# Optimization experiments

Hardware: AMD Instinct MI355X
Metric: run time of the kernel (lower is better)

The kernel has to match this reference:

```python
import jax, jax.numpy as jnp
import numpy as np

N, E, T, F, HID, NCLS = 50000, 800000, 6, 64, 48, 2
LN_EPS = 1e-5


def setup_inputs() -> dict:
    key = jax.random.key(0)
    ks = jax.random.split(key, 24)
    p = lambda k, shape, s=0.1: jax.random.normal(k, shape, dtype=jnp.float32) * s
    inp = {
        "x_seq": jax.random.normal(ks[0], (T, N, F), dtype=jnp.float32),
        "edge_index": jax.random.randint(ks[1], (2, E), 0, N, dtype=jnp.int64),
        "edge_weight": jax.random.uniform(ks[2], (E,), dtype=jnp.float32),
        # GCN layer 0
        "W0": p(ks[3], (F, HID)), "b0": jnp.zeros((HID,), jnp.float32),
        "g0": jnp.ones((HID,), jnp.float32), "be0": jnp.zeros((HID,), jnp.float32),
        # GCN layer 1
        "W1": p(ks[4], (HID, HID)), "b1": jnp.zeros((HID,), jnp.float32),
        "g1": jnp.ones((HID,), jnp.float32), "be1": jnp.zeros((HID,), jnp.float32),
        # GRU (torch gate order: r, z, n)
        "W_ih": p(ks[5], (3 * HID, HID)), "W_hh": p(ks[6], (3 * HID, HID)),
        "b_ih": jnp.zeros((3 * HID,), jnp.float32), "b_hh": jnp.zeros((3 * HID,), jnp.float32),
        # classifier MLP
        "Wc1": p(ks[7], (HID, HID // 2)), "bc1": jnp.zeros((HID // 2,), jnp.float32),
        "Wc2": p(ks[8], (HID // 2, NCLS)), "bc2": jnp.zeros((NCLS,), jnp.float32),
    }
    return inp


def _layer_norm(x, g, b):
    mu = x.mean(-1, keepdims=True)
    var = ((x - mu) ** 2).mean(-1, keepdims=True)
    return (x - mu) * jax.lax.rsqrt(var + LN_EPS) * g + b


def reference(x_seq, edge_index, edge_weight, W0, b0, g0, be0, W1, b1, g1, be1,
              W_ih, W_hh, b_ih, b_hh, Wc1, bc1, Wc2, bc2):
    n = x_seq.shape[1]
    hid = W0.shape[1]
    row, col = edge_index[0], edge_index[1]
    # PyG GCNConv default: add self-loops (weight 1), symmetric normalization
    loop = jnp.arange(n)
    row_f = jnp.concatenate([row, loop])
    col_f = jnp.concatenate([col, loop])
    w_f = jnp.concatenate([edge_weight, jnp.ones((n,), edge_weight.dtype)])
    deg = jax.ops.segment_sum(w_f, col_f, num_segments=n)
    dis = jnp.where(deg > 0, jax.lax.rsqrt(jnp.maximum(deg, 1e-12)), 0.0)
    norm = dis[row_f] * w_f * dis[col_f]  # [E+N]

    def gcn(x, W, b):
        h = x @ W                              # [N, hid]
        msg = h[row_f] * norm[:, None]         # [E+N, hid]
        return jax.ops.segment_sum(msg, col_f, num_segments=n) + b

    def spatial(x_t):
        # layer 0: no residual (in_dim != hid)
        h1 = jax.nn.relu(_layer_norm(gcn(x_t, W0, b0), g0, be0))
        # layer 1: residual (dropout is eval-mode no-op)
        h2 = jax.nn.relu(_layer_norm(gcn(h1, W1, b1), g1, be1)) + h1
        return h2

    # sequential map over T keeps per-step [E,hid] message buffers small
    H = jax.lax.map(spatial, x_seq)            # [T, N, hid]

    def gru_step(h, x_t):
        gi = x_t @ W_ih.T + b_ih               # [N, 3*hid]
        gh = h @ W_hh.T + b_hh
        i_r, i_z, i_n = jnp.split(gi, 3, axis=-1)
        h_r, h_z, h_n = jnp.split(gh, 3, axis=-1)
        r = jax.nn.sigmoid(i_r + h_r)
        z = jax.nn.sigmoid(i_z + h_z)
        nv = jnp.tanh(i_n + r * h_n)
        h_new = (1.0 - z) * nv + z * h
        return h_new, None

    h0 = jnp.zeros((n, hid), x_seq.dtype)
    z_last, _ = jax.lax.scan(gru_step, h0, H)  # last hidden state [N, hid]

    logits = jax.nn.relu(z_last @ Wc1 + bc1) @ Wc2 + bc2  # [N, 2]
    return logits
```

## Files before the change

kernel.cpp:

```cpp
#include <hip/hip_runtime.h>
#include <hip/hip_fp16.h>
#include <math.h>

#define NN 50000
#define NE 800000
#define TT 6
#define HID 48
#define NB 196

__device__ __forceinline__ float sigmoidf_(float x){ return 1.0f/(1.0f+__expf(-x)); }
__device__ __forceinline__ float tanhf_(float x){
  float xc = fminf(fmaxf(x,-15.f),15.f);
  float t = __expf(2.f*xc);
  return (t-1.f)/(t+1.f);
}
__device__ __forceinline__ unsigned f2bf(float x){
  unsigned u = __float_as_uint(x);
  return (u + 0x7fffu + ((u>>16)&1u)) >> 16;
}
__device__ __forceinline__ unsigned pack2(float a, float b){
  return f2bf(a) | (f2bf(b)<<16);
}
__device__ __forceinline__ float bflo(unsigned u){ return __uint_as_float(u<<16); }
__device__ __forceinline__ float bfhi(unsigned u){ return __uint_as_float(u & 0xffff0000u); }
__device__ __forceinline__ unsigned f2h(float x){
  return (unsigned)__half_as_ushort(__float2half(x));
}
__device__ __forceinline__ float h2f(unsigned u){
  return __half2float(__ushort_as_half((unsigned short)(u & 0xffffu)));
}
__device__ __forceinline__ unsigned pack2h(float a, float b){
  return f2h(a) | (f2h(b)<<16);
}

typedef __fp16 h2t __attribute__((ext_vector_type(2)));

__device__ __forceinline__ unsigned pkrtz(float a, float b){
#if __has_builtin(__builtin_amdgcn_cvt_pkrtz)
  auto r = __builtin_amdgcn_cvt_pkrtz(a, b);
  return __builtin_bit_cast(unsigned, r);
#else
  return pack2h(a, b);
#endif
}
__device__ __forceinline__ float dot2f(unsigned a, unsigned b, float c){
#if __has_builtin(__builtin_amdgcn_fdot2)
  return __builtin_amdgcn_fdot2(__builtin_bit_cast(h2t, a), __builtin_bit_cast(h2t, b), c, false);
#else
  h2t av = __builtin_bit_cast(h2t, a), bv = __builtin_bit_cast(h2t, b);
  return c + (float)av[0]*(float)bv[0] + (float)av[1]*(float)bv[1];
#endif
}

struct U3 { unsigned x,y,z; };

__device__ __forceinline__ int block_scan_incl(int x, int* wsum){
  int lane = threadIdx.x & 63, w = threadIdx.x >> 6;
  int v = x;
#pragma unroll
  for(int d=1; d<64; d<<=1){
    int u = __shfl_up(v, d, 64);
    if(lane >= d) v += u;
  }
  if(lane==63) wsum[w] = v;
  __syncthreads();
  int add = 0;
#pragma unroll
  for(int k=0;k<3;k++) if(w>k) add += wsum[k];
  return v + add;
}

__global__ __launch_bounds__(256) void k_setup(int* cnt,
                                               const float* __restrict__ Wih, const float* __restrict__ Whh,
                                               unsigned* Wall){
  int i = blockIdx.x*256+threadIdx.x;
  if(i<NN) cnt[i]=0;
  if(i < 6*24*48){
    int wv = i/1152, r = i%1152;
    int k2 = r/48, c = r%48;
    int cc = (c<24)? c : (c-24);
    int row = (cc<8) ? (wv*8 + cc) : (cc<16) ? (48 + wv*8 + cc-8) : (96 + wv*8 + cc-16);
    const float* Wsrc = (c<24)? Whh : Wih;
    Wall[i] = pack2h(Wsrc[row*48 + 2*k2], Wsrc[row*48 + 2*k2 + 1]);
  }
}

__global__ __launch_bounds__(256) void k_cnt(const int* __restrict__ ei, int* cnt, int* pos){
  int e = blockIdx.x*256+threadIdx.x;
  if(e<NE){
    int c = ei[NE+e];
    pos[e] = atomicAdd(&cnt[c], 1);
  }
}

__global__ __launch_bounds__(256) void k_partA(const int* __restrict__ cnt, int* bsum){
  __shared__ int wsum[4];
  int i = blockIdx.x*256+threadIdx.x;
  int x = (i<NN)? cnt[i] : 0;
  int lane = threadIdx.x & 63, w = threadIdx.x >> 6;
  int v = x;
#pragma unroll
  for(int m=32;m>=1;m>>=1) v += __shfl_xor(v, m, 64);
  if(lane==0) wsum[w]=v;
  __syncthreads();
  if(threadIdx.x==0) bsum[blockIdx.x] = wsum[0]+wsum[1]+wsum[2]+wsum[3];
}

__global__ __launch_bounds__(256) void k_midB(const int* __restrict__ bsum, int* bpre, int* offs){
  __shared__ int wsum[4];
  int t = threadIdx.x;
  int x = (t<NB)? bsum[t] : 0;
  int incl = block_scan_incl(x, wsum);
  if(t<NB) bpre[t] = incl - x;
  if(t==255) offs[NN] = incl;
}

__global__ __launch_bounds__(256) void k_offsC(const int* __restrict__ cnt, const int* __restrict__ bpre,
                                               int* offs){
  __shared__ int wsum[4];
  int i = blockIdx.x*256+threadIdx.x;
  int x = (i<NN)? cnt[i] : 0;
  int incl = block_scan_incl(x, wsum);
  if(i<NN) offs[i] = bpre[blockIdx.x] + incl - x;
}

__global__ __launch_bounds__(256) void k_scatter(const int* __restrict__ ei, const float* __restrict__ ew,
                                                 const int* __restrict__ offs, const int* __restrict__ pos,
                                                 int2* __restrict__ csr){
  int e = blockIdx.x*256+threadIdx.x;
  if(e<NE){
    int c = ei[NE+e];
    int2 v; v.x = ei[e]; v.y = __float_as_int(ew[e]);
    csr[offs[c]+pos[e]] = v;
  }
}

__global__ __launch_bounds__(256) void k_deg(const int2* __restrict__ csr, const int* __restrict__ offs,
                                             float* dis){
  int i = blockIdx.x*256+threadIdx.x;
  if(i<NN){
    float s = 1.f;
    int e0=offs[i], e1=offs[i+1];
    for(int j=e0;j<e1;j++) s += __int_as_float(csr[j].y);
    dis[i] = rsqrtf(s);
  }
}

__global__ __launch_bounds__(256) void k_normE(int2* __restrict__ csr, const float* __restrict__ dis){
  int j = blockIdx.x*256+threadIdx.x;
  if(j<NE){
    int2 v = csr[j];
    v.y = __float_as_int(dis[v.x]*__int_as_float(v.y));
    csr[j] = v;
  }
}

__global__ __launch_bounds__(256) void k_mm0(const float* __restrict__ X, const float* __restrict__ W,
                                             unsigned* __restrict__ A){
  int s = __builtin_amdgcn_readfirstlane(threadIdx.x>>6);
  int n = blockIdx.x*64 + (threadIdx.x&63);
  if(n>=NN) return;
  const float* xb = X + (long long)n*64;
  const float* wb = W + 12*s;
  float acc[TT][12];
#pragma unroll
  for(int t=0;t<TT;t++)
#pragma unroll
    for(int j=0;j<12;j++) acc[t][j]=0.f;
#pragma unroll
  for(int t=0;t<TT;t++){
    const float* xt = xb + (long long)t*NN*64;
#pragma unroll 2
    for(int k4=0;k4<16;k4++){
      float4 xv = *reinterpret_cast<const float4*>(xt + 4*k4);
#pragma unroll
      for(int q=0;q<4;q++){
        const float* wr = wb + (4*k4+q)*HID;
        float w[12];
#pragma unroll
        for(int j=0;j<12;j++) w[j]=wr[j];
        float xs = (&xv.x)[q];
#pragma unroll
        for(int j=0;j<12;j++) acc[t][j] = fmaf(xs, w[j], acc[t][j]);
      }
    }
  }
  unsigned buf[36];
#pragma unroll
  for(int j=0;j<12;j++){
    buf[3*j  ]=pack2(acc[0][j],acc[1][j]);
    buf[3*j+1]=pack2(acc[2][j],acc[3][j]);
    buf[3*j+2]=pack2(acc[4][j],acc[5][j]);
  }
  uint4* o4 = reinterpret_cast<uint4*>(A + (long long)n*144 + 36*s);
#pragma unroll
  for(int q=0;q<9;q++) o4[q] = make_uint4(buf[4*q],buf[4*q+1],buf[4*q+2],buf[4*q+3]);
}

__global__ __launch_bounds__(256) void k_mm1(const float* __restrict__ X, const float* __restrict__ W,
                                             unsigned* __restrict__ A){
  int s = __builtin_amdgcn_readfirstlane(threadIdx.x>>6);
  int n = blockIdx.x*64 + (threadIdx.x&63);
  if(n>=NN) return;
  const float* xb = X + (long long)n*(TT*HID);
  const float* wb = W + 12*s;
  float acc[TT][12];
#pragma unroll
  for(int t=0;t<TT;t++)
#pragma unroll
    for(int j=0;j<12;j++) acc[t][j]=0.f;
#pragma unroll
  for(int t=0;t<TT;t++){
    const float* xt = xb + t*HID;
#pragma unroll 2
    for(int k4=0;k4<12;k4++){
      float4 xv = *reinterpret_cast<const float4*>(xt + 4*k4);
#pragma unroll
      for(int q=0;q<4;q++){
        const float* wr = wb + (4*k4+q)*HID;
        float w[12];
#pragma unroll
        for(int j=0;j<12;j++) w[j]=wr[j];
        float xs = (&xv.x)[q];
#pragma unroll
        for(int j=0;j<12;j++) acc[t][j] = fmaf(xs, w[j], acc[t][j]);
      }
    }
  }
  unsigned buf[36];
#pragma unroll
  for(int j=0;j<12;j++){
    buf[3*j  ]=pack2(acc[0][j],acc[1][j]);
    buf[3*j+1]=pack2(acc[2][j],acc[3][j]);
    buf[3*j+2]=pack2(acc[4][j],acc[5][j]);
  }
  uint4* o4 = reinterpret_cast<uint4*>(A + (long long)n*144 + 36*s);
#pragma unroll
  for(int q=0;q<9;q++) o4[q] = make_uint4(buf[4*q],buf[4*q+1],buf[4*q+2],buf[4*q+3]);
}

__global__ __launch_bounds__(256) void k_agg(const unsigned* __restrict__ A, const float* __restrict__ bias,
                                             const float* __restrict__ gain, const float* __restrict__ beta,
                                             const float* __restrict__ resid, float* __restrict__ out,
                                             const int* __restrict__ offs, const int2* __restrict__ csr,
                                             const float* __restrict__ dis){
  int wid = (blockIdx.x*256+threadIdx.x)>>6;
  int lane = threadIdx.x & 63;
  if(wid>=NN) return;
  const bool act = lane<HID;
  const int f = act? lane : (HID-1);
  float dn = dis[wid];
  float acc[TT];
  {
    U3 v = *reinterpret_cast<const U3*>(A + (long long)wid*144 + 3*f);
    acc[0]=dn*bflo(v.x); acc[1]=dn*bfhi(v.x);
    acc[2]=dn*bflo(v.y); acc[3]=dn*bfhi(v.y);
    acc[4]=dn*bflo(v.z); acc[5]=dn*bfhi(v.z);
  }
  int e0=offs[wid], e1=offs[wid+1];
  int e=e0;
  for(; e+3<e1; e+=4){
    int2 i0=csr[e], i1=csr[e+1], i2=csr[e+2], i3=csr[e+3];
    U3 d0 = *reinterpret_cast<const U3*>(A + (long long)i0.x*144 + 3*f);
    U3 d1 = *reinterpret_cast<const U3*>(A + (long long)i1.x*144 + 3*f);
    U3 d2 = *reinterpret_cast<const U3*>(A + (long long)i2.x*144 + 3*f);
    U3 d3 = *reinterpret_cast<const U3*>(A + (long long)i3.x*144 + 3*f);
    float n0=__int_as_float(i0.y), n1=__int_as_float(i1.y);
    float n2=__int_as_float(i2.y), n3=__int_as_float(i3.y);
    acc[0]=fmaf(n0,bflo(d0.x),acc[0]); acc[1]=fmaf(n0,bfhi(d0.x),acc[1]);
    acc[2]=fmaf(n0,bflo(d0.y),acc[2]); acc[3]=fmaf(n0,bfhi(d0.y),acc[3]);
    acc[4]=fmaf(n0,bflo(d0.z),acc[4]); acc[5]=fmaf(n0,bfhi(d0.z),acc[5]);
    acc[0]=fmaf(n1,bflo(d1.x),acc[0]); acc[1]=fmaf(n1,bfhi(d1.x),acc[1]);
    acc[2]=fmaf(n1,bflo(d1.y),acc[2]); acc[3]=fmaf(n1,bfhi(d1.y),acc[3]);
    acc[4]=fmaf(n1,bflo(d1.z),acc[4]); acc[5]=fmaf(n1,bfhi(d1.z),acc[5]);
    acc[0]=fmaf(n2,bflo(d2.x),acc[0]); acc[1]=fmaf(n2,bfhi(d2.x),acc[1]);
    acc[2]=fmaf(n2,bflo(d2.y),acc[2]); acc[3]=fmaf(n2,bfhi(d2.y),acc[3]);
    acc[4]=fmaf(n2,bflo(d2.z),acc[4]); acc[5]=fmaf(n2,bfhi(d2.z),acc[5]);
    acc[0]=fmaf(n3,bflo(d3.x),acc[0]); acc[1]=fmaf(n3,bfhi(d3.x),acc[1]);
    acc[2]=fmaf(n3,bflo(d3.y),acc[2]); acc[3]=fmaf(n3,bfhi(d3.y),acc[3]);
    acc[4]=fmaf(n3,bflo(d3.z),acc[4]); acc[5]=fmaf(n3,bfhi(d3.z),acc[5]);
  }
  for(; e<e1; ++e){
    int2 i0=csr[e];
    U3 d0 = *reinterpret_cast<const U3*>(A + (long long)i0.x*144 + 3*f);
    float n0=__int_as_float(i0.y);
    acc[0]=fmaf(n0,bflo(d0.x),acc[0]); acc[1]=fmaf(n0,bfhi(d0.x),acc[1]);
    acc[2]=fmaf(n0,bflo(d0.y),acc[2]); acc[3]=fmaf(n0,bfhi(d0.y),acc[3]);
    acc[4]=fmaf(n0,bflo(d0.z),acc[4]); acc[5]=fmaf(n0,bfhi(d0.z),acc[5]);
  }
  float bb = bias[f], gg = gain[f], be = beta[f];
  const float rn = 1.0f/HID;
#pragma unroll
  for(int t=0;t<TT;t++){
    float val = fmaf(acc[t], dn, bb);
    float v = act? val : 0.f;
    float s = v, s2 = v*v;
#pragma unroll
    for(int m=32;m>=1;m>>=1){
      s  += __shfl_xor(s,  m, 64);
      s2 += __shfl_xor(s2, m, 64);
    }
    float mu  = s*rn;
    float var = fmaxf(s2*rn - mu*mu, 0.f);
    float y = (val-mu)*rsqrtf(var+1e-5f)*gg + be;
    y = fmaxf(y, 0.f);
    long long oidx = (long long)wid*(TT*HID) + t*HID + f;
    if(resid) y += resid[oidx];
    if(act) out[oidx] = y;
  }
}

__global__ __launch_bounds__(384) void k_gruF2(const float* __restrict__ X,
                                               const unsigned* __restrict__ Wall,
                                               const float* __restrict__ bih, const float* __restrict__ bhh,
                                               const float* __restrict__ Wc1, const float* __restrict__ bc1,
                                               const float* __restrict__ Wc2, const float* __restrict__ bc2,
                                               float* __restrict__ out){
  __shared__ unsigned xall[TT*24*64];
  __shared__ unsigned hb[2][24*64];
  int tid = threadIdx.x;
  int wv = __builtin_amdgcn_readfirstlane(tid>>6);
  int lane = tid & 63;
  int f0 = wv*8;
  long long n = (long long)blockIdx.x*64 + lane;
  long long gn = (n<NN)? n : (NN-1);

  {
    const float* xb = X + gn*(TT*HID) + wv*HID;
#pragma unroll
    for(int q=0;q<12;q++){
      float4 v = *reinterpret_cast<const float4*>(xb + 4*q);
      xall[(wv*24 + 2*q  )*64 + lane] = pkrtz(v.x, v.y);
      xall[(wv*24 + 2*q+1)*64 + lane] = pkrtz(v.z, v.w);
    }
  }
  for(int i=tid;i<24*64;i+=384) hb[0][i]=0u;

  float rb[8], zb[8], nbi[8], nbh[8], hprev[8];
#pragma unroll
  for(int j=0;j<8;j++){
    rb[j] = bih[f0+j]    + bhh[f0+j];
    zb[j] = bih[48+f0+j] + bhh[48+f0+j];
    nbi[j]= bih[96+f0+j];
    nbh[j]= bhh[96+f0+j];
    hprev[j]=0.f;
  }
  __syncthreads();

  int cur=0;
  for(int t=0;t<TT;t++){
    float acc[24], accn[8];
#pragma unroll
    for(int j=0;j<8;j++){ acc[j]=rb[j]; acc[8+j]=zb[j]; acc[16+j]=nbh[j]; accn[j]=nbi[j]; }
    const unsigned* hbc = &hb[cur][0];
    const unsigned* xtc = &xall[t*24*64];
#pragma unroll 2
    for(int k2=0;k2<24;k2++){
      const unsigned* wp = Wall + (wv*24+k2)*48;
      unsigned ws[48];
#pragma unroll
      for(int q=0;q<48;q++) ws[q]=wp[q];
      unsigned h2k = hbc[k2*64+lane];
      unsigned xk  = xtc[k2*64+lane];
#pragma unroll
      for(int c=0;c<24;c++) acc[c]  = dot2f(h2k, ws[c],    acc[c]);
#pragma unroll
      for(int c=0;c<16;c++) acc[c]  = dot2f(xk,  ws[24+c], acc[c]);
#pragma unroll
      for(int c=0;c<8;c++)  accn[c] = dot2f(xk,  ws[40+c], accn[c]);
    }
    unsigned* hw = &hb[cur^1][0];
    float hn[8];
#pragma unroll
    for(int j=0;j<8;j++){
      float r  = sigmoidf_(acc[j]);
      float zg = sigmoidf_(acc[8+j]);
      float ng = tanhf_(accn[j] + r*acc[16+j]);
      float hv = (1.f-zg)*ng + zg*hprev[j];
      hprev[j]=hv; hn[j]=hv;
    }
#pragma unroll
    for(int m=0;m<4;m++) hw[(wv*4+m)*64+lane] = pack2h(hn[2*m], hn[2*m+1]);
    __syncthreads();
    cur^=1;
  }

  if(wv==0 && n<NN){
    const unsigned* hbc=&hb[cur][0];
    float hv[24];
#pragma unroll
    for(int j=0;j<24;j++) hv[j]=bc1[j];
#pragma unroll 2
    for(int k2=0;k2<24;k2++){
      unsigned u = hbc[k2*64+lane];
      float hk0 = h2f(u), hk1 = h2f(u>>16);
      const float* w0 = Wc1 + (2*k2)*24;
      const float* w1 = Wc1 + (2*k2+1)*24;
#pragma unroll
      for(int j=0;j<24;j++) hv[j] = fmaf(hk0, w0[j], hv[j]);
#pragma unroll
      for(int j=0;j<24;j++) hv[j] = fmaf(hk1, w1[j], hv[j]);
    }
    float l0=bc2[0], l1=bc2[1];
#pragma unroll
    for(int j=0;j<24;j++){
      float a = fmaxf(hv[j],0.f);
      l0 = fmaf(a, Wc2[2*j],   l0);
      l1 = fmaf(a, Wc2[2*j+1], l1);
    }
    reinterpret_cast<float2*>(out)[n] = make_float2(l0,l1);
  }
}

static inline size_t al256(size_t x){ return (x+255)&~(size_t)255; }

extern "C" void kernel_launch(void* const* d_in, const int* in_sizes, int n_in,
                              void* d_out, int out_size, void* d_ws, size_t ws_size,
                              hipStream_t stream){
  const float* x_seq=(const float*)d_in[0];
  const int*   ei   =(const int*)d_in[1];
  const float* ew   =(const float*)d_in[2];
  const float* W0=(const float*)d_in[3];  const float* b0=(const float*)d_in[4];
  const float* g0=(const float*)d_in[5];  const float* be0=(const float*)d_in[6];
  const float* W1=(const float*)d_in[7];  const float* b1=(const float*)d_in[8];
  const float* g1=(const float*)d_in[9];  const float* be1=(const float*)d_in[10];
  const float* Wih=(const float*)d_in[11];const float* Whh=(const float*)d_in[12];
  const float* bih=(const float*)d_in[13];const float* bhh=(const float*)d_in[14];
  const float* Wc1=(const float*)d_in[15];const float* bc1=(const float*)d_in[16];
  const float* Wc2=(const float*)d_in[17];const float* bc2=(const float*)d_in[18];
  float* outp=(float*)d_out;

  char* p=(char*)d_ws; size_t off=0;
  auto alloc=[&](size_t bytes)->void*{ void* r=p+off; off=al256(off+bytes); return r; };
  float* dis    =(float*)alloc((size_t)NN*4);
  int*   cnt    =(int*)  alloc((size_t)NN*4);
  int*   offs   =(int*)  alloc((size_t)(NN+1)*4);
  int*   bsum   =(int*)  alloc((size_t)NB*4);
  int*   bpre   =(int*)  alloc((size_t)NB*4);
  int*   pos    =(int*)  alloc((size_t)NE*4);
  int2*  csr    =(int2*) alloc((size_t)NE*8);
  unsigned* Wall=(unsigned*)alloc((size_t)6*24*48*4);
  unsigned* A   =(unsigned*)alloc((size_t)NN*576 + 1024);
  float* h1     =(float*)alloc((size_t)NN*TT*HID*4);
  float* h2     =(float*)alloc((size_t)NN*TT*HID*4);

  const int GN=(NN+255)/256, GE=(NE+255)/256;
  const int GMM=(NN+63)/64;
  const int GAGG=(NN*64+255)/256;
  const int GGRU=(NN+63)/64;

  k_setup  <<<GN,256,0,stream>>>(cnt,Wih,Whh,Wall);
  k_cnt    <<<GE,256,0,stream>>>(ei,cnt,pos);
  k_partA  <<<NB,256,0,stream>>>(cnt,bsum);
  k_midB   <<<1,256,0,stream>>>(bsum,bpre,offs);
  k_offsC  <<<NB,256,0,stream>>>(cnt,bpre,offs);
  k_scatter<<<GE,256,0,stream>>>(ei,ew,offs,pos,csr);
  k_deg    <<<GN,256,0,stream>>>(csr,offs,dis);
  k_normE  <<<GE,256,0,stream>>>(csr,dis);

  k_mm0<<<GMM,256,0,stream>>>(x_seq, W0, A);
  k_agg<<<GAGG,256,0,stream>>>(A,b0,g0,be0,nullptr,h1,offs,csr,dis);
  k_mm1<<<GMM,256,0,stream>>>(h1, W1, A);
  k_agg<<<GAGG,256,0,stream>>>(A,b1,g1,be1,h1,h2,offs,csr,dis);
  k_gruF2<<<GGRU,384,0,stream>>>(h2, Wall, bih,bhh, Wc1,bc1,Wc2,bc2, outp);
}
```

Before: 635.1 us.

## Split GRU across 12 waves and precompute input gates off the recurrence

```diff
diff --git a/kernel.cpp b/kernel.cpp
--- a/kernel.cpp
+++ b/kernel.cpp
@@ -72,16 +72,16 @@
 
 __global__ __launch_bounds__(256) void k_setup(int* cnt,
                                                const float* __restrict__ Wih, const float* __restrict__ Whh,
-                                               unsigned* Wall){
+                                               unsigned* W2){
   int i = blockIdx.x*256+threadIdx.x;
   if(i<NN) cnt[i]=0;
-  if(i < 6*24*48){
-    int wv = i/1152, r = i%1152;
-    int k2 = r/48, c = r%48;
-    int cc = (c<24)? c : (c-24);
-    int row = (cc<8) ? (wv*8 + cc) : (cc<16) ? (48 + wv*8 + cc-8) : (96 + wv*8 + cc-16);
-    const float* Wsrc = (c<24)? Whh : Wih;
-    Wall[i] = pack2h(Wsrc[row*48 + 2*k2], Wsrc[row*48 + 2*k2 + 1]);
+  if(i < 12*24*24){
+    int w = i/576, r = i%576;
+    int k2 = r/24, c = r%24;
+    int cc = (c<12)? c : (c-12);
+    int row = (cc<4) ? (w*4 + cc) : (cc<8) ? (48 + w*4 + cc-4) : (96 + w*4 + cc-8);
+    const float* Wsrc = (c<12)? Whh : Wih;
+    W2[i] = pack2h(Wsrc[row*48 + 2*k2], Wsrc[row*48 + 2*k2 + 1]);
   }
 }
 
@@ -310,8 +310,8 @@
   }
 }
 
-__global__ __launch_bounds__(384) void k_gruF2(const float* __restrict__ X,
-                                               const unsigned* __restrict__ Wall,
+__global__ __launch_bounds__(768) void k_gruF4(const float* __restrict__ X,
+                                               const unsigned* __restrict__ W2,
                                                const float* __restrict__ bih, const float* __restrict__ bhh,
                                                const float* __restrict__ Wc1, const float* __restrict__ bc1,
                                                const float* __restrict__ Wc2, const float* __restrict__ bc2,
@@ -321,68 +321,89 @@
   int tid = threadIdx.x;
   int wv = __builtin_amdgcn_readfirstlane(tid>>6);
   int lane = tid & 63;
-  int f0 = wv*8;
+  int f0 = wv*4;
   long long n = (long long)blockIdx.x*64 + lane;
-  long long gn = (n<NN)? n : (NN-1);
 
   {
-    const float* xb = X + gn*(TT*HID) + wv*HID;
-#pragma unroll
-    for(int q=0;q<12;q++){
-      float4 v = *reinterpret_cast<const float4*>(xb + 4*q);
-      xall[(wv*24 + 2*q  )*64 + lane] = pkrtz(v.x, v.y);
-      xall[(wv*24 + 2*q+1)*64 + lane] = pkrtz(v.z, v.w);
-    }
-  }
-  for(int i=tid;i<24*64;i+=384) hb[0][i]=0u;
-
-  float rb[8], zb[8], nbi[8], nbh[8], hprev[8];
-#pragma unroll
-  for(int j=0;j<8;j++){
-    rb[j] = bih[f0+j]    + bhh[f0+j];
-    zb[j] = bih[48+f0+j] + bhh[48+f0+j];
-    nbi[j]= bih[96+f0+j];
-    nbh[j]= bhh[96+f0+j];
+    int nd = tid/12, q = tid-12*nd;
+    long long g = (long long)blockIdx.x*64+nd; if(g>NN-1) g=NN-1;
+    const float* xs = X + g*(TT*HID) + 4*q;
+#pragma unroll
+    for(int t=0;t<TT;t++){
+      float4 v = *reinterpret_cast<const float4*>(xs + t*HID);
+      xall[(t*24 + 2*q  )*64 + nd] = pkrtz(v.x, v.y);
+      xall[(t*24 + 2*q+1)*64 + nd] = pkrtz(v.z, v.w);
+    }
+  }
+  for(int i=tid;i<24*64;i+=768) hb[0][i]=0u;
+
+  float rbi[4], zbi[4], nbi[4], rbh[4], zbh[4], nbh[4], hprev[4];
+#pragma unroll
+  for(int j=0;j<4;j++){
+    rbi[j]=bih[f0+j]; zbi[j]=bih[48+f0+j]; nbi[j]=bih[96+f0+j];
+    rbh[j]=bhh[f0+j]; zbh[j]=bhh[48+f0+j]; nbh[j]=bhh[96+f0+j];
     hprev[j]=0.f;
   }
   __syncthreads();
 
   int cur=0;
-  for(int t=0;t<TT;t++){
-    float acc[24], accn[8];
-#pragma unroll
-    for(int j=0;j<8;j++){ acc[j]=rb[j]; acc[8+j]=zb[j]; acc[16+j]=nbh[j]; accn[j]=nbi[j]; }
-    const unsigned* hbc = &hb[cur][0];
-    const unsigned* xtc = &xall[t*24*64];
+#pragma unroll
+  for(int tp=0; tp<2; tp++){
+    unsigned gi[18];
+#pragma unroll
+    for(int s=0;s<3;s++){
+      float a[12];
+#pragma unroll
+      for(int j=0;j<4;j++){ a[j]=rbi[j]; a[4+j]=zbi[j]; a[8+j]=nbi[j]; }
+      const unsigned* xtc = &xall[(tp*3+s)*24*64];
 #pragma unroll 2
-    for(int k2=0;k2<24;k2++){
-      const unsigned* wp = Wall + (wv*24+k2)*48;
-      unsigned ws[48];
-#pragma unroll
-      for(int q=0;q<48;q++) ws[q]=wp[q];
-      unsigned h2k = hbc[k2*64+lane];
-      unsigned xk  = xtc[k2*64+lane];
-#pragma unroll
-      for(int c=0;c<24;c++) acc[c]  = dot2f(h2k, ws[c],    acc[c]);
-#pragma unroll
-      for(int c=0;c<16;c++) acc[c]  = dot2f(xk,  ws[24+c], acc[c]);
-#pragma unroll
-      for(int c=0;c<8;c++)  accn[c] = dot2f(xk,  ws[40+c], accn[c]);
-    }
-    unsigned* hw = &hb[cur^1][0];
-    float hn[8];
-#pragma unroll
-    for(int j=0;j<8;j++){
-      float r  = sigmoidf_(acc[j]);
-      float zg = sigmoidf_(acc[8+j]);
-      float ng = tanhf_(accn[j] + r*acc[16+j]);
-      float hv = (1.f-zg)*ng + zg*hprev[j];
-      hprev[j]=hv; hn[j]=hv;
-    }
-#pragma unroll
-    for(int m=0;m<4;m++) hw[(wv*4+m)*64+lane] = pack2h(hn[2*m], hn[2*m+1]);
-    __syncthreads();
-    cur^=1;
+      for(int k2=0;k2<24;k2++){
+        const unsigned* wp = W2 + (wv*24+k2)*24 + 12;
+        unsigned ws[12];
+#pragma unroll
+        for(int q=0;q<12;q++) ws[q]=wp[q];
+        unsigned xk = xtc[k2*64+lane];
+#pragma unroll
+        for(int c=0;c<12;c++) a[c]=dot2f(xk, ws[c], a[c]);
+      }
+#pragma unroll
+      for(int m=0;m<6;m++) gi[s*6+m]=pack2h(a[2*m], a[2*m+1]);
+    }
+#pragma unroll
+    for(int s=0;s<3;s++){
+      float acc[12];
+#pragma unroll
+      for(int j=0;j<4;j++){ acc[j]=rbh[j]; acc[4+j]=zbh[j]; acc[8+j]=nbh[j]; }
+      const unsigned* hbc = &hb[cur][0];
+#pragma unroll 2
+      for(int k2=0;k2<24;k2++){
+        const unsigned* wp = W2 + (wv*24+k2)*24;
+        unsigned ws[12];
+#pragma unroll
+        for(int q=0;q<12;q++) ws[q]=wp[q];
+        unsigned h2k = hbc[k2*64+lane];
+#pragma unroll
+        for(int c=0;c<12;c++) acc[c]=dot2f(h2k, ws[c], acc[c]);
+      }
+      unsigned* hw = &hb[cur^1][0];
+      float hn[4];
+#pragma unroll
+      for(int j=0;j<4;j++){
+        unsigned pr=gi[s*6+(j>>1)], pz=gi[s*6+2+(j>>1)], pn=gi[s*6+4+(j>>1)];
+        float gir=(j&1)? h2f(pr>>16):h2f(pr);
+        float giz=(j&1)? h2f(pz>>16):h2f(pz);
+        float gin=(j&1)? h2f(pn>>16):h2f(pn);
+        float r  = sigmoidf_(acc[j]+gir);
+        float zg = sigmoidf_(acc[4+j]+giz);
+        float ng = tanhf_(gin + r*acc[8+j]);
+        float hv = (1.f-zg)*ng + zg*hprev[j];
+        hprev[j]=hv; hn[j]=hv;
+      }
+      hw[(2*wv  )*64+lane] = pack2h(hn[0],hn[1]);
+      hw[(2*wv+1)*64+lane] = pack2h(hn[2],hn[3]);
+      __syncthreads();
+      cur^=1;
+    }
   }
 
   if(wv==0 && n<NN){
@@ -439,7 +460,7 @@
   int*   bpre   =(int*)  alloc((size_t)NB*4);
   int*   pos    =(int*)  alloc((size_t)NE*4);
   int2*  csr    =(int2*) alloc((size_t)NE*8);
-  unsigned* Wall=(unsigned*)alloc((size_t)6*24*48*4);
+  unsigned* W2  =(unsigned*)alloc((size_t)12*24*24*4);
   unsigned* A   =(unsigned*)alloc((size_t)NN*576 + 1024);
   float* h1     =(float*)alloc((size_t)NN*TT*HID*4);
   float* h2     =(float*)alloc((size_t)NN*TT*HID*4);
@@ -449,7 +470,7 @@
   const int GAGG=(NN*64+255)/256;
   const int GGRU=(NN+63)/64;
 
-  k_setup  <<<GN,256,0,stream>>>(cnt,Wih,Whh,Wall);
+  k_setup  <<<GN,256,0,stream>>>(cnt,Wih,Whh,W2);
   k_cnt    <<<GE,256,0,stream>>>(ei,cnt,pos);
   k_partA  <<<NB,256,0,stream>>>(cnt,bsum);
   k_midB   <<<1,256,0,stream>>>(bsum,bpre,offs);
@@ -462,5 +483,5 @@
   k_agg<<<GAGG,256,0,stream>>>(A,b0,g0,be0,nullptr,h1,offs,csr,dis);
   k_mm1<<<GMM,256,0,stream>>>(h1, W1, A);
   k_agg<<<GAGG,256,0,stream>>>(A,b1,g1,be1,h1,h2,offs,csr,dis);
-  k_gruF2<<<GGRU,384,0,stream>>>(h2, Wall, bih,bhh, Wc1,bc1,Wc2,bc2, outp);
-}
+  k_gruF4<<<GGRU,768,0,stream>>>(h2, W2, bih,bhh, Wc1,bc1,Wc2,bc2, outp);
+}
```

New measurement: 614.1 us. 1.03x faster.
